# Performance work log

Measured on AMD Instinct MI355X. Metric: run time of the kernel, lower is better.

The kernel has to match this reference:

```python
import jax, jax.numpy as jnp
import numpy as np

T, BS, IN, H = 2048, 64, 256, 512  # seq_len, batch, inputSize, hiddenSize


def setup_inputs() -> dict:
    key = jax.random.key(0)
    k1, k2, k3, k4 = jax.random.split(key, 4)
    std = 1.0 / np.sqrt(H)
    return {
        "x": jax.random.normal(k1, (T, BS, IN), dtype=jnp.float32),
        "Wi": jax.random.uniform(k2, (IN, 4 * H), dtype=jnp.float32, minval=-std, maxval=std),
        "Wh": jax.random.uniform(k3, (H, 4 * H), dtype=jnp.float32, minval=-std, maxval=std),
        "B": jax.random.uniform(k4, (4 * H,), dtype=jnp.float32, minval=-std, maxval=std),
    }


def reference(x, Wi, Wh, B):
    # Precompute the non-recurrent input projection once: [T, BS, 4H]
    xW = jnp.einsum("tbi,ig->tbg", x, Wi) + B
    h0 = jnp.zeros((BS, H), dtype=x.dtype)
    c0 = jnp.zeros((BS, H), dtype=x.dtype)

    def step(carry, xw_t):
        h, c = carry
        gates = xw_t + h @ Wh  # [BS, 4H]
        i = jax.nn.sigmoid(gates[:, :H])
        f = jax.nn.sigmoid(gates[:, H:2 * H])
        g = jnp.tanh(gates[:, 2 * H:3 * H])
        o = jax.nn.sigmoid(gates[:, 3 * H:])
        c_new = f * c + i * g
        h_new = o * jnp.tanh(c_new)
        return (h_new, c_new), h_new

    (hT, cT), out = jax.lax.scan(step, (h0, c0), xW)
    return out, (hT, cT)
```

## Files before the change

kernel.cpp:

```cpp
#include <hip/hip_runtime.h>

typedef _Float16 half8 __attribute__((ext_vector_type(8)));
typedef _Float16 half4v __attribute__((ext_vector_type(4)));
typedef float f32x4 __attribute__((ext_vector_type(4)));

#define T_LEN 2048
#define BSZ   64
#define INSZ  256
#define HSZ   512
#define G4H   2048

#define OFF_XW   0ULL
#define OFF_X16  536870912ULL
#define OFF_WIT  603979776ULL
#define OFF_WHT  605028352ULL
#define OFF_HBUF 607125504ULL
#define OFF_CTR  607256576ULL

__device__ __forceinline__ float fast_rcp(float x) { return __builtin_amdgcn_rcpf(x); }
__device__ __forceinline__ float sigm(float x)  { return fast_rcp(1.f + __expf(-x)); }
__device__ __forceinline__ float tanhf_(float x){ return 1.f - 2.f * fast_rcp(1.f + __expf(2.f * x)); }

__global__ void convert_x(const float* __restrict__ x, _Float16* __restrict__ x16, int n4) {
    int i = blockIdx.x * blockDim.x + threadIdx.x;
    int stride = gridDim.x * blockDim.x;
    const float4* xv = (const float4*)x;
    for (; i < n4; i += stride) {
        float4 v = xv[i];
        half4v h;
        h[0] = (_Float16)v.x; h[1] = (_Float16)v.y;
        h[2] = (_Float16)v.z; h[3] = (_Float16)v.w;
        *(half4v*)(x16 + (size_t)i * 4) = h;
    }
}

__global__ void transpose_w(const float* __restrict__ W, _Float16* __restrict__ WT, int K) {
    int id = blockIdx.x * blockDim.x + threadIdx.x;
    int total = K * G4H, stride = gridDim.x * blockDim.x;
    for (; id < total; id += stride) {
        int k = id >> 11;
        int n = id & 2047;
        WT[(size_t)n * K + k] = (_Float16)W[id];
    }
}

__global__ void init_state(unsigned* __restrict__ hbuf_u, unsigned* __restrict__ ctr) {
    int id = blockIdx.x * blockDim.x + threadIdx.x;
    if (id < 32768) hbuf_u[id] = 0u;
    if (id < 128)   ctr[id] = 0u;
}

__global__ __launch_bounds__(256) void gemm_xw(const _Float16* __restrict__ A,
                                               const _Float16* __restrict__ Bt,
                                               const float* __restrict__ bias,
                                               _Float16* __restrict__ C) {
    __shared__ __align__(16) _Float16 As[128 * 32];
    __shared__ __align__(16) _Float16 Bs[128 * 32];
    const int tid  = threadIdx.x;
    const int w    = tid >> 6;
    const int l    = tid & 63;
    const int lo   = l & 15;
    const int quad = l >> 4;
    const int rowBase = blockIdx.y * 128;
    const int colBase = blockIdx.x * 128;
    const int wr = (w >> 1) * 64, wc = (w & 1) * 64;

    f32x4 acc[4][4] = {};

    const int v0 = tid, v1 = tid + 256;
    for (int kt = 0; kt < 8; kt++) {
        ((half8*)As)[v0] = *(const half8*)(A + (size_t)(rowBase + (v0 >> 2)) * INSZ + kt * 32 + (v0 & 3) * 8);
        ((half8*)As)[v1] = *(const half8*)(A + (size_t)(rowBase + (v1 >> 2)) * INSZ + kt * 32 + (v1 & 3) * 8);
        ((half8*)Bs)[v0] = *(const half8*)(Bt + (size_t)(colBase + (v0 >> 2)) * INSZ + kt * 32 + (v0 & 3) * 8);
        ((half8*)Bs)[v1] = *(const half8*)(Bt + (size_t)(colBase + (v1 >> 2)) * INSZ + kt * 32 + (v1 & 3) * 8);
        __syncthreads();
        half8 af[4], bf[4];
#pragma unroll
        for (int mt = 0; mt < 4; mt++)
            af[mt] = *(const half8*)(As + (wr + mt * 16 + lo) * 32 + quad * 8);
#pragma unroll
        for (int nt = 0; nt < 4; nt++)
            bf[nt] = *(const half8*)(Bs + (wc + nt * 16 + lo) * 32 + quad * 8);
#pragma unroll
        for (int mt = 0; mt < 4; mt++)
#pragma unroll
            for (int nt = 0; nt < 4; nt++)
                acc[mt][nt] = __builtin_amdgcn_mfma_f32_16x16x32_f16(af[mt], bf[nt], acc[mt][nt], 0, 0, 0);
        __syncthreads();
    }

#pragma unroll
    for (int nt = 0; nt < 4; nt++) {
        int col = colBase + wc + nt * 16 + lo;
        float bv = bias[col];
#pragma unroll
        for (int mt = 0; mt < 4; mt++) {
#pragma unroll
            for (int r = 0; r < 4; r++) {
                int row = rowBase + wr + mt * 16 + quad * 4 + r;
                C[(size_t)row * G4H + col] = (_Float16)(acc[mt][nt][r] + bv);
            }
        }
    }
}

#define CBLK 8
__global__ __launch_bounds__(256, 1) void lstm_scan(const _Float16* __restrict__ xw,
                                                    const _Float16* __restrict__ whT,
                                                    _Float16* __restrict__ hbuf,
                                                    unsigned* __restrict__ ctr,
                                                    float* __restrict__ out) {
    __shared__ __align__(16) _Float16 ldsW[2 * 16 * 256 * 8];
    half8* ldsF = (half8*)ldsW;

    const int tid  = threadIdx.x;
    const int w    = tid >> 6;
    const int l    = tid & 63;
    const int lo   = l & 15;
    const int quad = l >> 4;
    const int g = blockIdx.x & 3;
    const int j = blockIdx.x >> 2;
    const int col = j * 64 + w * 16 + lo;
    const int sr0 = quad * 4;
    const int bglob = g * 16;

#pragma unroll
    for (int qq = 0; qq < 2; qq++) {
        const _Float16* wrow = whT + (size_t)((qq + 2) * HSZ + col) * HSZ + quad * 8;
#pragma unroll
        for (int kt = 0; kt < 16; kt++)
            ldsF[(qq * 16 + kt) * 256 + tid] = *(const half8*)(wrow + kt * 32);
    }

    half8 bfrag[2][16];
#pragma unroll
    for (int q = 0; q < 2; q++) {
        const _Float16* wrow = whT + (size_t)(q * HSZ + col) * HSZ + quad * 8;
#pragma unroll
        for (int kt = 0; kt < 16; kt++)
            bfrag[q][kt] = *(const half8*)(wrow + kt * 32);
    }

    float creg[4] = {0.f, 0.f, 0.f, 0.f};

    float xpre[4][4];
#pragma unroll
    for (int q = 0; q < 4; q++)
#pragma unroll
        for (int r = 0; r < 4; r++)
            xpre[q][r] = (float)xw[(size_t)(bglob + sr0 + r) * G4H + q * HSZ + col];

    unsigned* myctr = ctr + g * 32;

    for (int t = 0; t < T_LEN; t++) {
        const int rb = t & 1, wb = rb ^ 1;

        const _Float16* hrow = hbuf + rb * (BSZ * HSZ) + (size_t)(bglob + lo) * HSZ + quad * 8;
        half8 af[16];
#pragma unroll
        for (int kt = 0; kt < 16; kt++) af[kt] = *(const half8*)(hrow + kt * 32);

        f32x4 acc[4];
#pragma unroll
        for (int q = 0; q < 4; q++) {
            acc[q][0] = xpre[q][0]; acc[q][1] = xpre[q][1];
            acc[q][2] = xpre[q][2]; acc[q][3] = xpre[q][3];
        }
#pragma unroll
        for (int kt = 0; kt < 16; kt++) {
            acc[0] = __builtin_amdgcn_mfma_f32_16x16x32_f16(af[kt], bfrag[0][kt], acc[0], 0, 0, 0);
            acc[1] = __builtin_amdgcn_mfma_f32_16x16x32_f16(af[kt], bfrag[1][kt], acc[1], 0, 0, 0);
            half8 b2 = ldsF[kt * 256 + tid];
            half8 b3 = ldsF[(16 + kt) * 256 + tid];
            acc[2] = __builtin_amdgcn_mfma_f32_16x16x32_f16(af[kt], b2, acc[2], 0, 0, 0);
            acc[3] = __builtin_amdgcn_mfma_f32_16x16x32_f16(af[kt], b3, acc[3], 0, 0, 0);
        }

        if (t + 1 < T_LEN) {
#pragma unroll
            for (int q = 0; q < 4; q++)
#pragma unroll
                for (int r = 0; r < 4; r++)
                    xpre[q][r] = (float)xw[((size_t)(t + 1) * BSZ + bglob + sr0 + r) * G4H + q * HSZ + col];
        }

#pragma unroll
        for (int r = 0; r < 4; r++) {
            float iv = sigm(acc[0][r]);
            float fv = sigm(acc[1][r]);
            float gv = tanhf_(acc[2][r]);
            float ov = sigm(acc[3][r]);
            float cn = fv * creg[r] + iv * gv;
            creg[r] = cn;
            float hn = ov * tanhf_(cn);
            const size_t brow = (size_t)(bglob + sr0 + r);
            hbuf[wb * (BSZ * HSZ) + brow * HSZ + col] = (_Float16)hn;
            __builtin_nontemporal_store(hn, out + ((size_t)t * BSZ + brow) * HSZ + col);
            if (t == T_LEN - 1) {
                __builtin_nontemporal_store(hn, out + (size_t)T_LEN * BSZ * HSZ + brow * HSZ + col);
                __builtin_nontemporal_store(cn, out + (size_t)T_LEN * BSZ * HSZ + (size_t)BSZ * HSZ + brow * HSZ + col);
            }
        }

        __syncthreads();
        if (tid == 0) {
            __threadfence();
            __hip_atomic_fetch_add(myctr, 1u, __ATOMIC_RELAXED, __HIP_MEMORY_SCOPE_AGENT);
            const unsigned target = (unsigned)(CBLK * (t + 1));
            while (__hip_atomic_load(myctr, __ATOMIC_RELAXED, __HIP_MEMORY_SCOPE_AGENT) < target)
                ;
            __threadfence();
        }
        __syncthreads();
    }
}

extern "C" void kernel_launch(void* const* d_in, const int* in_sizes, int n_in,
                              void* d_out, int out_size, void* d_ws, size_t ws_size,
                              hipStream_t stream) {
    const float* x  = (const float*)d_in[0];
    const float* Wi = (const float*)d_in[1];
    const float* Wh = (const float*)d_in[2];
    const float* B  = (const float*)d_in[3];
    float* out = (float*)d_out;

    char* ws = (char*)d_ws;
    _Float16* xW   = (_Float16*)(ws + OFF_XW);
    _Float16* x16  = (_Float16*)(ws + OFF_X16);
    _Float16* WiT  = (_Float16*)(ws + OFF_WIT);
    _Float16* WhT  = (_Float16*)(ws + OFF_WHT);
    _Float16* hbuf = (_Float16*)(ws + OFF_HBUF);
    unsigned* ctr  = (unsigned*)(ws + OFF_CTR);

    hipLaunchKernelGGL(convert_x, dim3(4096), dim3(256), 0, stream, x, x16, 8388608);
    hipLaunchKernelGGL(transpose_w, dim3(512), dim3(256), 0, stream, Wi, WiT, INSZ);
    hipLaunchKernelGGL(transpose_w, dim3(1024), dim3(256), 0, stream, Wh, WhT, HSZ);
    hipLaunchKernelGGL(init_state, dim3(128), dim3(256), 0, stream, (unsigned*)hbuf, ctr);
    hipLaunchKernelGGL(gemm_xw, dim3(16, 1024), dim3(256), 0, stream, x16, WiT, B, xW);
    hipLaunchKernelGGL(lstm_scan, dim3(32), dim3(256), 0, stream, xW, WhT, hbuf, ctr, out);
}
```

Before: 11.23 ms.

## Pipeline four batch groups per block with per-slot flag sync and prefetch

The scan kernel drops from 32 blocks to 8. Each block now covers all four 16-row batch groups in rotating slots. A shared atomic-counter barrier is replaced by per-block flag stores and polled coherent loads, and the h and xW fragments for the next slot are prefetched while the current slot's MFMAs run. The intent is to hide the inter-block synchronization latency and global-load latency on the sequential critical path. In exchange, each block does four times the matrix work per timestep, and correctness now depends on hand-written cache-bypass asm and waitcnt ordering.

```diff
diff --git a/kernel.cpp b/kernel.cpp
--- a/kernel.cpp
+++ b/kernel.cpp
@@ -20,6 +20,35 @@
 __device__ __forceinline__ float fast_rcp(float x) { return __builtin_amdgcn_rcpf(x); }
 __device__ __forceinline__ float sigm(float x)  { return fast_rcp(1.f + __expf(-x)); }
 __device__ __forceinline__ float tanhf_(float x){ return 1.f - 2.f * fast_rcp(1.f + __expf(2.f * x)); }
+
+template<int OFF>
+__device__ __forceinline__ half8 ldg_coh_b128(const _Float16* p) {
+    half8 r;
+    asm volatile("global_load_dwordx4 %0, %1, off offset:%2 sc0 sc1"
+                 : "=v"(r) : "v"(p), "n"(OFF));
+    return r;
+}
+template<int OFF>
+__device__ __forceinline__ unsigned ldg_u16(const _Float16* p) {
+    unsigned r;
+    asm volatile("global_load_ushort %0, %1, off offset:%2"
+                 : "=v"(r) : "v"(p), "n"(OFF));
+    return r;
+}
+__device__ __forceinline__ unsigned ldg_coh_u32(const unsigned* p) {
+    unsigned r;
+    asm volatile("global_load_dword %0, %1, off sc0 sc1" : "=v"(r) : "v"(p));
+    return r;
+}
+__device__ __forceinline__ void stg_short_sc(_Float16* p, unsigned v) {
+    asm volatile("global_store_short %0, %1, off sc0 sc1" :: "v"(p), "v"(v));
+}
+__device__ __forceinline__ void stg_dword_nt(float* p, float v) {
+    asm volatile("global_store_dword %0, %1, off nt" :: "v"(p), "v"(v));
+}
+__device__ __forceinline__ void stg_dword_sc(unsigned* p, unsigned v) {
+    asm volatile("global_store_dword %0, %1, off sc0 sc1" :: "v"(p), "v"(v));
+}
 
 __global__ void convert_x(const float* __restrict__ x, _Float16* __restrict__ x16, int n4) {
     int i = blockIdx.x * blockDim.x + threadIdx.x;
@@ -46,8 +75,8 @@
 
 __global__ void init_state(unsigned* __restrict__ hbuf_u, unsigned* __restrict__ ctr) {
     int id = blockIdx.x * blockDim.x + threadIdx.x;
-    if (id < 32768) hbuf_u[id] = 0u;
-    if (id < 128)   ctr[id] = 0u;
+    if (id < 32768) __hip_atomic_store(hbuf_u + id, 0u, __ATOMIC_RELAXED, __HIP_MEMORY_SCOPE_AGENT);
+    if (id < 128)   __hip_atomic_store(ctr + id, 0u, __ATOMIC_RELAXED, __HIP_MEMORY_SCOPE_AGENT);
 }
 
 __global__ __launch_bounds__(256) void gemm_xw(const _Float16* __restrict__ A,
@@ -104,7 +133,6 @@
     }
 }
 
-#define CBLK 8
 __global__ __launch_bounds__(256, 1) void lstm_scan(const _Float16* __restrict__ xw,
                                                     const _Float16* __restrict__ whT,
                                                     _Float16* __restrict__ hbuf,
@@ -118,11 +146,9 @@
     const int l    = tid & 63;
     const int lo   = l & 15;
     const int quad = l >> 4;
-    const int g = blockIdx.x & 3;
-    const int j = blockIdx.x >> 2;
-    const int col = j * 64 + w * 16 + lo;
-    const int sr0 = quad * 4;
-    const int bglob = g * 16;
+    const int j    = blockIdx.x;
+    const int col  = j * 64 + w * 16 + lo;
+    const int sr0  = quad * 4;
 
 #pragma unroll
     for (int qq = 0; qq < 2; qq++) {
@@ -131,7 +157,6 @@
         for (int kt = 0; kt < 16; kt++)
             ldsF[(qq * 16 + kt) * 256 + tid] = *(const half8*)(wrow + kt * 32);
     }
-
     half8 bfrag[2][16];
 #pragma unroll
     for (int q = 0; q < 2; q++) {
@@ -140,78 +165,134 @@
         for (int kt = 0; kt < 16; kt++)
             bfrag[q][kt] = *(const half8*)(wrow + kt * 32);
     }
-
-    float creg[4] = {0.f, 0.f, 0.f, 0.f};
-
-    float xpre[4][4];
-#pragma unroll
-    for (int q = 0; q < 4; q++)
-#pragma unroll
-        for (int r = 0; r < 4; r++)
-            xpre[q][r] = (float)xw[(size_t)(bglob + sr0 + r) * G4H + q * HSZ + col];
-
-    unsigned* myctr = ctr + g * 32;
+    __syncthreads();
+
+    float creg[4][4]  = {};
+    float hlast[4][4] = {};
+    half8 afA[16], afB[16];
+    unsigned xqA[16], xqB[16];
+    unsigned pkA = 0, pkB = 0;
+#pragma unroll
+    for (int kt = 0; kt < 16; kt++) { half8 z = {}; afA[kt] = z; }
+
+#define AF_LOAD16(DST, P)                                                   \
+    DST[0]  = ldg_coh_b128<0>(P);   DST[1]  = ldg_coh_b128<64>(P);          \
+    DST[2]  = ldg_coh_b128<128>(P); DST[3]  = ldg_coh_b128<192>(P);         \
+    DST[4]  = ldg_coh_b128<256>(P); DST[5]  = ldg_coh_b128<320>(P);         \
+    DST[6]  = ldg_coh_b128<384>(P); DST[7]  = ldg_coh_b128<448>(P);         \
+    DST[8]  = ldg_coh_b128<512>(P); DST[9]  = ldg_coh_b128<576>(P);         \
+    DST[10] = ldg_coh_b128<640>(P); DST[11] = ldg_coh_b128<704>(P);         \
+    DST[12] = ldg_coh_b128<768>(P); DST[13] = ldg_coh_b128<832>(P);         \
+    DST[14] = ldg_coh_b128<896>(P); DST[15] = ldg_coh_b128<960>(P);
+
+#define XQ_LOAD(DST, XB)                                                    \
+    { const _Float16 *x0_ = (XB), *x1_ = (XB) + G4H,                        \
+                     *x2_ = (XB) + 2 * G4H, *x3_ = (XB) + 3 * G4H;          \
+      DST[0]  = ldg_u16<0>(x0_);    DST[4]  = ldg_u16<1024>(x0_);           \
+      DST[8]  = ldg_u16<2048>(x0_); DST[12] = ldg_u16<3072>(x0_);           \
+      DST[1]  = ldg_u16<0>(x1_);    DST[5]  = ldg_u16<1024>(x1_);           \
+      DST[9]  = ldg_u16<2048>(x1_); DST[13] = ldg_u16<3072>(x1_);           \
+      DST[2]  = ldg_u16<0>(x2_);    DST[6]  = ldg_u16<1024>(x2_);           \
+      DST[10] = ldg_u16<2048>(x2_); DST[14] = ldg_u16<3072>(x2_);           \
+      DST[3]  = ldg_u16<0>(x3_);    DST[7]  = ldg_u16<1024>(x3_);           \
+      DST[11] = ldg_u16<2048>(x3_); DST[15] = ldg_u16<3072>(x3_); }
+
+    {
+        const _Float16* xb0 = xw + (size_t)sr0 * G4H + col;
+        XQ_LOAD(xqA, xb0)
+        asm volatile("s_waitcnt vmcnt(0)");
+        __builtin_amdgcn_sched_barrier(0);
+    }
+
+#define SLOT(G, AFU, AFL, XQU, XQL, PKU, PKL)                               \
+{                                                                           \
+    constexpr int g_ = (G);                                                 \
+    const int gn_ = (g_ + 1) & 3;                                           \
+    const int tn_ = (g_ == 3) ? t + 1 : t;                                  \
+        \
+    if (tn_ > 0 && tn_ < T_LEN) {                                           \
+        const unsigned need_ = (unsigned)tn_;                               \
+        const unsigned* pa_ = ctr + gn_ * 32 + (l & 7);                     \
+        while (!__all((int)(PKU >= need_))) {                               \
+            PKU = ldg_coh_u32(pa_);                                         \
+            asm volatile("s_waitcnt vmcnt(0)");                             \
+            __builtin_amdgcn_sched_barrier(0);                              \
+        }                                                                   \
+    }                                                                       \
+       \
+    if (tn_ < T_LEN) {                                                      \
+        const _Float16* hr_ = hbuf + (size_t)((tn_ - 1) & 1) * (BSZ * HSZ)  \
+                              + (size_t)(gn_ * 16 + lo) * HSZ + quad * 8;   \
+        AF_LOAD16(AFL, hr_)                                                 \
+        const _Float16* xb_ = xw + ((size_t)tn_ * BSZ + gn_ * 16 + sr0) * G4H + col; \
+        XQ_LOAD(XQL, xb_)                                                   \
+    }                                                                       \
+            \
+    f32x4 acc[4];                                                           \
+    _Pragma("unroll")                                                       \
+    for (int q_ = 0; q_ < 4; q_++) {                                        \
+        _Pragma("unroll")                                                   \
+        for (int r_ = 0; r_ < 4; r_++)                                      \
+            acc[q_][r_] = (float)__builtin_bit_cast(_Float16, (unsigned short)XQU[q_ * 4 + r_]); \
+    }                                                                       \
+    _Pragma("unroll")                                                       \
+    for (int kt_ = 0; kt_ < 16; kt_++) {                                    \
+        acc[0] = __builtin_amdgcn_mfma_f32_16x16x32_f16(AFU[kt_], bfrag[0][kt_], acc[0], 0, 0, 0); \
+        acc[1] = __builtin_amdgcn_mfma_f32_16x16x32_f16(AFU[kt_], bfrag[1][kt_], acc[1], 0, 0, 0); \
+        half8 b2_ = ldsF[kt_ * 256 + tid];                                  \
+        half8 b3_ = ldsF[(16 + kt_) * 256 + tid];                           \
+        acc[2] = __builtin_amdgcn_mfma_f32_16x16x32_f16(AFU[kt_], b2_, acc[2], 0, 0, 0); \
+        acc[3] = __builtin_amdgcn_mfma_f32_16x16x32_f16(AFU[kt_], b3_, acc[3], 0, 0, 0); \
+    }                                                                       \
+     \
+    if (((g_ >= 2) ? t + 1 : t) < T_LEN)                                    \
+        PKL = ldg_coh_u32(ctr + ((g_ + 2) & 3) * 32 + (l & 7));             \
+     \
+    _Pragma("unroll")                                                       \
+    for (int r_ = 0; r_ < 4; r_++) {                                        \
+        float iv = sigm(acc[0][r_]);                                        \
+        float fv = sigm(acc[1][r_]);                                        \
+        float gv = tanhf_(acc[2][r_]);                                      \
+        float ov = sigm(acc[3][r_]);                                        \
+        float cn = fv * creg[g_][r_] + iv * gv;                             \
+        creg[g_][r_] = cn;                                                  \
+        float hn = ov * tanhf_(cn);                                         \
+        hlast[g_][r_] = hn;                                                 \
+        const size_t brow_ = (size_t)(g_ * 16 + sr0 + r_);                  \
+        stg_short_sc(hbuf + (size_t)(t & 1) * (BSZ * HSZ) + brow_ * HSZ + col, \
+                     (unsigned)__builtin_bit_cast(unsigned short, (_Float16)hn)); \
+        stg_dword_nt(out + ((size_t)t * BSZ + brow_) * HSZ + col, hn);      \
+    }                                                                       \
+     \
+    asm volatile("s_waitcnt vmcnt(8)");                                     \
+    __builtin_amdgcn_sched_barrier(0);                                      \
+    __builtin_amdgcn_s_barrier();                                           \
+     \
+    if (!(t == 0 && g_ == 0) && tid == 0) {                                 \
+        stg_dword_sc(ctr + ((g_ + 3) & 3) * 32 + j,                         \
+                     (unsigned)(((g_ == 0) ? t - 1 : t) + 1));              \
+    }                                                                       \
+}
 
     for (int t = 0; t < T_LEN; t++) {
-        const int rb = t & 1, wb = rb ^ 1;
-
-        const _Float16* hrow = hbuf + rb * (BSZ * HSZ) + (size_t)(bglob + lo) * HSZ + quad * 8;
-        half8 af[16];
-#pragma unroll
-        for (int kt = 0; kt < 16; kt++) af[kt] = *(const half8*)(hrow + kt * 32);
-
-        f32x4 acc[4];
-#pragma unroll
-        for (int q = 0; q < 4; q++) {
-            acc[q][0] = xpre[q][0]; acc[q][1] = xpre[q][1];
-            acc[q][2] = xpre[q][2]; acc[q][3] = xpre[q][3];
+        SLOT(0, afA, afB, xqA, xqB, pkA, pkB)
+        SLOT(1, afB, afA, xqB, xqA, pkB, pkA)
+        SLOT(2, afA, afB, xqA, xqB, pkA, pkB)
+        SLOT(3, afB, afA, xqB, xqA, pkB, pkA)
+    }
+
+#undef SLOT
+#undef AF_LOAD16
+#undef XQ_LOAD
+
+#pragma unroll
+    for (int g = 0; g < 4; g++) {
+#pragma unroll
+        for (int r = 0; r < 4; r++) {
+            const size_t brow = (size_t)(g * 16 + sr0 + r);
+            out[(size_t)T_LEN * BSZ * HSZ + brow * HSZ + col] = hlast[g][r];
+            out[(size_t)T_LEN * BSZ * HSZ + (size_t)BSZ * HSZ + brow * HSZ + col] = creg[g][r];
         }
-#pragma unroll
-        for (int kt = 0; kt < 16; kt++) {
-            acc[0] = __builtin_amdgcn_mfma_f32_16x16x32_f16(af[kt], bfrag[0][kt], acc[0], 0, 0, 0);
-            acc[1] = __builtin_amdgcn_mfma_f32_16x16x32_f16(af[kt], bfrag[1][kt], acc[1], 0, 0, 0);
-            half8 b2 = ldsF[kt * 256 + tid];
-            half8 b3 = ldsF[(16 + kt) * 256 + tid];
-            acc[2] = __builtin_amdgcn_mfma_f32_16x16x32_f16(af[kt], b2, acc[2], 0, 0, 0);
-            acc[3] = __builtin_amdgcn_mfma_f32_16x16x32_f16(af[kt], b3, acc[3], 0, 0, 0);
-        }
-
-        if (t + 1 < T_LEN) {
-#pragma unroll
-            for (int q = 0; q < 4; q++)
-#pragma unroll
-                for (int r = 0; r < 4; r++)
-                    xpre[q][r] = (float)xw[((size_t)(t + 1) * BSZ + bglob + sr0 + r) * G4H + q * HSZ + col];
-        }
-
-#pragma unroll
-        for (int r = 0; r < 4; r++) {
-            float iv = sigm(acc[0][r]);
-            float fv = sigm(acc[1][r]);
-            float gv = tanhf_(acc[2][r]);
-            float ov = sigm(acc[3][r]);
-            float cn = fv * creg[r] + iv * gv;
-            creg[r] = cn;
-            float hn = ov * tanhf_(cn);
-            const size_t brow = (size_t)(bglob + sr0 + r);
-            hbuf[wb * (BSZ * HSZ) + brow * HSZ + col] = (_Float16)hn;
-            __builtin_nontemporal_store(hn, out + ((size_t)t * BSZ + brow) * HSZ + col);
-            if (t == T_LEN - 1) {
-                __builtin_nontemporal_store(hn, out + (size_t)T_LEN * BSZ * HSZ + brow * HSZ + col);
-                __builtin_nontemporal_store(cn, out + (size_t)T_LEN * BSZ * HSZ + (size_t)BSZ * HSZ + brow * HSZ + col);
-            }
-        }
-
-        __syncthreads();
-        if (tid == 0) {
-            __threadfence();
-            __hip_atomic_fetch_add(myctr, 1u, __ATOMIC_RELAXED, __HIP_MEMORY_SCOPE_AGENT);
-            const unsigned target = (unsigned)(CBLK * (t + 1));
-            while (__hip_atomic_load(myctr, __ATOMIC_RELAXED, __HIP_MEMORY_SCOPE_AGENT) < target)
-                ;
-            __threadfence();
-        }
-        __syncthreads();
     }
 }
 
@@ -237,5 +318,5 @@
     hipLaunchKernelGGL(transpose_w, dim3(1024), dim3(256), 0, stream, Wh, WhT, HSZ);
     hipLaunchKernelGGL(init_state, dim3(128), dim3(256), 0, stream, (unsigned*)hbuf, ctr);
     hipLaunchKernelGGL(gemm_xw, dim3(16, 1024), dim3(256), 0, stream, x16, WiT, B, xW);
-    hipLaunchKernelGGL(lstm_scan, dim3(32), dim3(256), 0, stream, xW, WhT, hbuf, ctr, out);
-}
+    hipLaunchKernelGGL(lstm_scan, dim3(8), dim3(256), 0, stream, xW, WhT, hbuf, ctr, out);
+}
```

After: 30.42 ms. +170.8%, slower.

## Replace block barrier with per-wave flag synchronization and coherent inline-asm loads

Applied to the files above, without the earlier changes.

Replaces the per-step __syncthreads plus single-thread atomic counter barrier with per-wave flag words. Each wave publishes its step number with a system-coherent store, and every wave polls all 32 flags of its batch group using a wave-wide __all. Hidden-state loads and stores now use sc0 sc1 coherent inline assembly, and the next step's xW prefetch is issued after the output stores with explicit waitcnt control. The aim is to shorten the critical path of the recurrent barrier, at the cost of more polling traffic and hand-written memory ordering that could be fragile.

```diff
diff --git a/kernel.cpp b/kernel.cpp
--- a/kernel.cpp
+++ b/kernel.cpp
@@ -20,6 +20,35 @@
 __device__ __forceinline__ float fast_rcp(float x) { return __builtin_amdgcn_rcpf(x); }
 __device__ __forceinline__ float sigm(float x)  { return fast_rcp(1.f + __expf(-x)); }
 __device__ __forceinline__ float tanhf_(float x){ return 1.f - 2.f * fast_rcp(1.f + __expf(2.f * x)); }
+
+template<int OFF>
+__device__ __forceinline__ half8 ldg_coh_b128(const _Float16* p) {
+    half8 r;
+    asm volatile("global_load_dwordx4 %0, %1, off offset:%2 sc0 sc1"
+                 : "=v"(r) : "v"(p), "n"(OFF));
+    return r;
+}
+template<int OFF>
+__device__ __forceinline__ unsigned ldg_u16(const _Float16* p) {
+    unsigned r;
+    asm volatile("global_load_ushort %0, %1, off offset:%2"
+                 : "=v"(r) : "v"(p), "n"(OFF));
+    return r;
+}
+__device__ __forceinline__ unsigned ldg_coh_u32(const unsigned* p) {
+    unsigned r;
+    asm volatile("global_load_dword %0, %1, off sc0 sc1" : "=v"(r) : "v"(p));
+    return r;
+}
+__device__ __forceinline__ void stg_short_sc(_Float16* p, unsigned v) {
+    asm volatile("global_store_short %0, %1, off sc0 sc1" :: "v"(p), "v"(v));
+}
+__device__ __forceinline__ void stg_dword_nt(float* p, float v) {
+    asm volatile("global_store_dword %0, %1, off nt" :: "v"(p), "v"(v));
+}
+__device__ __forceinline__ void stg_dword_sc(unsigned* p, unsigned v) {
+    asm volatile("global_store_dword %0, %1, off sc0 sc1" :: "v"(p), "v"(v));
+}
 
 __global__ void convert_x(const float* __restrict__ x, _Float16* __restrict__ x16, int n4) {
     int i = blockIdx.x * blockDim.x + threadIdx.x;
@@ -46,8 +75,8 @@
 
 __global__ void init_state(unsigned* __restrict__ hbuf_u, unsigned* __restrict__ ctr) {
     int id = blockIdx.x * blockDim.x + threadIdx.x;
-    if (id < 32768) hbuf_u[id] = 0u;
-    if (id < 128)   ctr[id] = 0u;
+    if (id < 32768) __hip_atomic_store(hbuf_u + id, 0u, __ATOMIC_RELAXED, __HIP_MEMORY_SCOPE_AGENT);
+    if (id < 128)   __hip_atomic_store(ctr + id, 0u, __ATOMIC_RELAXED, __HIP_MEMORY_SCOPE_AGENT);
 }
 
 __global__ __launch_bounds__(256) void gemm_xw(const _Float16* __restrict__ A,
@@ -104,7 +133,6 @@
     }
 }
 
-#define CBLK 8
 __global__ __launch_bounds__(256, 1) void lstm_scan(const _Float16* __restrict__ xw,
                                                     const _Float16* __restrict__ whT,
                                                     _Float16* __restrict__ hbuf,
@@ -118,10 +146,10 @@
     const int l    = tid & 63;
     const int lo   = l & 15;
     const int quad = l >> 4;
-    const int g = blockIdx.x & 3;
-    const int j = blockIdx.x >> 2;
-    const int col = j * 64 + w * 16 + lo;
-    const int sr0 = quad * 4;
+    const int g    = blockIdx.x & 3;
+    const int j    = blockIdx.x >> 2;
+    const int col  = j * 64 + w * 16 + lo;
+    const int sr0  = quad * 4;
     const int bglob = g * 16;
 
 #pragma unroll
@@ -131,7 +159,6 @@
         for (int kt = 0; kt < 16; kt++)
             ldsF[(qq * 16 + kt) * 256 + tid] = *(const half8*)(wrow + kt * 32);
     }
-
     half8 bfrag[2][16];
 #pragma unroll
     for (int q = 0; q < 2; q++) {
@@ -140,32 +167,69 @@
         for (int kt = 0; kt < 16; kt++)
             bfrag[q][kt] = *(const half8*)(wrow + kt * 32);
     }
+    __syncthreads();
 
     float creg[4] = {0.f, 0.f, 0.f, 0.f};
-
-    float xpre[4][4];
-#pragma unroll
-    for (int q = 0; q < 4; q++)
-#pragma unroll
-        for (int r = 0; r < 4; r++)
-            xpre[q][r] = (float)xw[(size_t)(bglob + sr0 + r) * G4H + q * HSZ + col];
-
-    unsigned* myctr = ctr + g * 32;
+    half8 af[16];
+    unsigned xq[16];
+    unsigned pk = 0;
+    const unsigned* pa = ctr + g * 32 + (l & 31);
+
+#define AF_LOAD16(DST, P)                                                   \
+    DST[0]  = ldg_coh_b128<0>(P);   DST[1]  = ldg_coh_b128<64>(P);          \
+    DST[2]  = ldg_coh_b128<128>(P); DST[3]  = ldg_coh_b128<192>(P);         \
+    DST[4]  = ldg_coh_b128<256>(P); DST[5]  = ldg_coh_b128<320>(P);         \
+    DST[6]  = ldg_coh_b128<384>(P); DST[7]  = ldg_coh_b128<448>(P);         \
+    DST[8]  = ldg_coh_b128<512>(P); DST[9]  = ldg_coh_b128<576>(P);         \
+    DST[10] = ldg_coh_b128<640>(P); DST[11] = ldg_coh_b128<704>(P);         \
+    DST[12] = ldg_coh_b128<768>(P); DST[13] = ldg_coh_b128<832>(P);         \
+    DST[14] = ldg_coh_b128<896>(P); DST[15] = ldg_coh_b128<960>(P);
+
+#define XQ_LOAD(DST, XB)                                                    \
+    { const _Float16 *x0_ = (XB), *x1_ = (XB) + G4H,                        \
+                     *x2_ = (XB) + 2 * G4H, *x3_ = (XB) + 3 * G4H;          \
+      DST[0]  = ldg_u16<0>(x0_);    DST[4]  = ldg_u16<1024>(x0_);           \
+      DST[8]  = ldg_u16<2048>(x0_); DST[12] = ldg_u16<3072>(x0_);           \
+      DST[1]  = ldg_u16<0>(x1_);    DST[5]  = ldg_u16<1024>(x1_);           \
+      DST[9]  = ldg_u16<2048>(x1_); DST[13] = ldg_u16<3072>(x1_);           \
+      DST[2]  = ldg_u16<0>(x2_);    DST[6]  = ldg_u16<1024>(x2_);           \
+      DST[10] = ldg_u16<2048>(x2_); DST[14] = ldg_u16<3072>(x2_);           \
+      DST[3]  = ldg_u16<0>(x3_);    DST[7]  = ldg_u16<1024>(x3_);           \
+      DST[11] = ldg_u16<2048>(x3_); DST[15] = ldg_u16<3072>(x3_); }
+
+    {
+        const _Float16* xb0 = xw + (size_t)(bglob + sr0) * G4H + col;
+        XQ_LOAD(xq, xb0)
+        asm volatile("s_waitcnt vmcnt(0)");
+        __builtin_amdgcn_sched_barrier(0);
+    }
 
     for (int t = 0; t < T_LEN; t++) {
         const int rb = t & 1, wb = rb ^ 1;
 
-        const _Float16* hrow = hbuf + rb * (BSZ * HSZ) + (size_t)(bglob + lo) * HSZ + quad * 8;
-        half8 af[16];
-#pragma unroll
-        for (int kt = 0; kt < 16; kt++) af[kt] = *(const half8*)(hrow + kt * 32);
+        if (t > 0) {
+            asm volatile("s_waitcnt vmcnt(20)");
+            __builtin_amdgcn_sched_barrier(0);
+            while (!__all((int)(pk >= (unsigned)t))) {
+                pk = ldg_coh_u32(pa);
+                asm volatile("s_waitcnt vmcnt(0)");
+                __builtin_amdgcn_sched_barrier(0);
+            }
+        }
+
+        const _Float16* hrow = hbuf + (size_t)rb * (BSZ * HSZ)
+                               + (size_t)(bglob + lo) * HSZ + quad * 8;
+        AF_LOAD16(af, hrow)
+        asm volatile("s_waitcnt vmcnt(0)");
+        __builtin_amdgcn_sched_barrier(0);
 
         f32x4 acc[4];
 #pragma unroll
-        for (int q = 0; q < 4; q++) {
-            acc[q][0] = xpre[q][0]; acc[q][1] = xpre[q][1];
-            acc[q][2] = xpre[q][2]; acc[q][3] = xpre[q][3];
-        }
+        for (int q = 0; q < 4; q++)
+#pragma unroll
+            for (int r = 0; r < 4; r++)
+                acc[q][r] = (float)__builtin_bit_cast(_Float16, (unsigned short)xq[q * 4 + r]);
+
 #pragma unroll
         for (int kt = 0; kt < 16; kt++) {
             acc[0] = __builtin_amdgcn_mfma_f32_16x16x32_f16(af[kt], bfrag[0][kt], acc[0], 0, 0, 0);
@@ -176,14 +240,7 @@
             acc[3] = __builtin_amdgcn_mfma_f32_16x16x32_f16(af[kt], b3, acc[3], 0, 0, 0);
         }
 
-        if (t + 1 < T_LEN) {
-#pragma unroll
-            for (int q = 0; q < 4; q++)
-#pragma unroll
-                for (int r = 0; r < 4; r++)
-                    xpre[q][r] = (float)xw[((size_t)(t + 1) * BSZ + bglob + sr0 + r) * G4H + q * HSZ + col];
-        }
-
+        float hnv[4];
 #pragma unroll
         for (int r = 0; r < 4; r++) {
             float iv = sigm(acc[0][r]);
@@ -193,26 +250,40 @@
             float cn = fv * creg[r] + iv * gv;
             creg[r] = cn;
             float hn = ov * tanhf_(cn);
+            hnv[r] = hn;
             const size_t brow = (size_t)(bglob + sr0 + r);
-            hbuf[wb * (BSZ * HSZ) + brow * HSZ + col] = (_Float16)hn;
-            __builtin_nontemporal_store(hn, out + ((size_t)t * BSZ + brow) * HSZ + col);
-            if (t == T_LEN - 1) {
-                __builtin_nontemporal_store(hn, out + (size_t)T_LEN * BSZ * HSZ + brow * HSZ + col);
-                __builtin_nontemporal_store(cn, out + (size_t)T_LEN * BSZ * HSZ + (size_t)BSZ * HSZ + brow * HSZ + col);
+            stg_short_sc(hbuf + (size_t)wb * (BSZ * HSZ) + brow * HSZ + col,
+                         (unsigned)__builtin_bit_cast(unsigned short, (_Float16)hn));
+        }
+
+        asm volatile("s_waitcnt vmcnt(0)");
+        __builtin_amdgcn_sched_barrier(0);
+        if (l == 0)
+            stg_dword_sc(ctr + g * 32 + j * 4 + w, (unsigned)(t + 1));
+
+        pk = ldg_coh_u32(pa);
+
+#pragma unroll
+        for (int r = 0; r < 4; r++) {
+            const size_t brow = (size_t)(bglob + sr0 + r);
+            stg_dword_nt(out + ((size_t)t * BSZ + brow) * HSZ + col, hnv[r]);
+        }
+        if (t == T_LEN - 1) {
+#pragma unroll
+            for (int r = 0; r < 4; r++) {
+                const size_t brow = (size_t)(bglob + sr0 + r);
+                out[(size_t)T_LEN * BSZ * HSZ + brow * HSZ + col] = hnv[r];
+                out[(size_t)T_LEN * BSZ * HSZ + (size_t)BSZ * HSZ + brow * HSZ + col] = creg[r];
             }
         }
-
-        __syncthreads();
-        if (tid == 0) {
-            __threadfence();
-            __hip_atomic_fetch_add(myctr, 1u, __ATOMIC_RELAXED, __HIP_MEMORY_SCOPE_AGENT);
-            const unsigned target = (unsigned)(CBLK * (t + 1));
-            while (__hip_atomic_load(myctr, __ATOMIC_RELAXED, __HIP_MEMORY_SCOPE_AGENT) < target)
-                ;
-            __threadfence();
-        }
-        __syncthreads();
-    }
+        if (t + 1 < T_LEN) {
+            const _Float16* xb = xw + ((size_t)(t + 1) * BSZ + bglob + sr0) * G4H + col;
+            XQ_LOAD(xq, xb)
+        }
+    }
+
+#undef AF_LOAD16
+#undef XQ_LOAD
 }
 
 extern "C" void kernel_launch(void* const* d_in, const int* in_sizes, int n_in,
```

After: 11.48 ms. 1.02x slower.
